# Kernel optimization log

Hardware: AMD Instinct MI355X
Metric: run time of the kernel (lower is better)

Reference implementation:

```python
import jax, jax.numpy as jnp
import numpy as np

B, S, T, H, E = 256, 512, 16, 1024, 512  # batch, src_len, trg_steps, hidden, emb_dim


def setup_inputs() -> dict:
    key = jax.random.key(0)
    ks = jax.random.split(key, 10)
    rn = lambda k, sh: jax.random.normal(k, sh, dtype=jnp.float32) * 0.05
    return {
        "trg_emb": rn(ks[0], (B, T, E)),
        "h0": rn(ks[1], (B, H)),
        "c0": rn(ks[2], (B, H)),
        "ctx": rn(ks[3], (B, S, H)),
        "src_len": jax.random.randint(ks[4], (B,), 1, S + 1, dtype=jnp.int32),
        "W_ih": rn(ks[5], (4 * H, E + H)),  # input-feeding: lstm in = emb + hidden
        "W_hh": rn(ks[6], (4 * H, H)),
        "b_ih": jnp.zeros((4 * H,), jnp.float32),
        "b_hh": jnp.zeros((4 * H,), jnp.float32),
        "W_in": rn(ks[7], (H, H)),    # attention linear_in (no bias)
        "W_out": rn(ks[8], (H, 2 * H)),  # attention linear_out (no bias)
    }


def reference(trg_emb, h0, c0, ctx, src_len, W_ih, W_hh, b_ih, b_hh, W_in, W_out):
    # mask[b, s] = s < src_len[b]
    mask = jnp.arange(S)[None, :] < src_len[:, None]  # (B, S)
    neg = jnp.float32(-1e9)

    def step(carry, emb_t):
        h, c, h_tilde = carry  # each (B, H); emb_t (B, E)
        # input feeding: concat target embedding with previous attentional vector
        x = jnp.concatenate([emb_t, h_tilde], axis=1)  # (B, E+H)
        gates = x @ W_ih.T + b_ih + h @ W_hh.T + b_hh  # (B, 4H), pytorch gate order i,f,g,o
        i, f, g, o = jnp.split(gates, 4, axis=1)
        i = jax.nn.sigmoid(i); f = jax.nn.sigmoid(f)
        g = jnp.tanh(g);       o = jax.nn.sigmoid(o)
        c = f * c + i * g
        h = o * jnp.tanh(c)
        # Luong soft-dot attention with src_len masking
        target = h @ W_in.T                                # (B, H)
        scores = jnp.einsum('bsh,bh->bs', ctx, target)     # (B, S)
        scores = jnp.where(mask, scores, neg)
        attn = jax.nn.softmax(scores, axis=-1)
        weighted = jnp.einsum('bs,bsh->bh', attn, ctx)     # (B, H)
        h_tilde = jnp.tanh(jnp.concatenate([weighted, h], axis=1) @ W_out.T)
        return (h, c, h_tilde), h_tilde

    # initial h_tilde = init_hidden[0] (per the original code)
    (h_f, c_f, _), hs = jax.lax.scan(step, (h0, c0, h0), jnp.swapaxes(trg_emb, 0, 1))
    output = jnp.swapaxes(hs, 0, 1)  # (B, T, H)
    return output, h_f, c_f
```

## Files before the change

kernel.cpp:

```cpp
#include <hip/hip_runtime.h>
#include <cstdint>
#include <cstddef>


#define B_ 256
#define S_ 512
#define T_ 16
#define H_ 1024
#define E_ 512

typedef unsigned short u16;
using short8 = __attribute__((ext_vector_type(8))) short;
using f32x4  = __attribute__((ext_vector_type(4))) float;

__device__ __forceinline__ float bf2f(u16 u) {
  union { uint32_t i; float f; } v; v.i = ((uint32_t)u) << 16; return v.f;
}
__device__ __forceinline__ u16 f2bf(float f) {
  union { uint32_t i; float f; } v; v.f = f;
  uint32_t r = v.i + 0x7fffu + ((v.i >> 16) & 1u);
  return (u16)(r >> 16);
}
__device__ __forceinline__ float sigmoidf_(float x) { return 1.f / (1.f + __expf(-x)); }

__device__ __forceinline__ void gload_lds16(const void* g, void* l) {
  __builtin_amdgcn_global_load_lds(
      (const __attribute__((address_space(1))) void*)g,
      (__attribute__((address_space(3))) void*)l, 16, 0, 0);
}

__global__ __launch_bounds__(256) void cvt_bf16(const float4* __restrict__ src,
                                                ushort4* __restrict__ dst, int n4) {
  for (int i = blockIdx.x * 256 + threadIdx.x; i < n4; i += gridDim.x * 256) {
    float4 v = src[i];
    ushort4 o; o.x = f2bf(v.x); o.y = f2bf(v.y); o.z = f2bf(v.z); o.w = f2bf(v.w);
    dst[i] = o;
  }
}

__global__ __launch_bounds__(256) void init_state(const float* __restrict__ h0,
                                                  const float* __restrict__ c0,
                                                  float* __restrict__ h32,
                                                  float* __restrict__ c,
                                                  u16* __restrict__ hbf,
                                                  u16* __restrict__ htbf) {
  int idx = blockIdx.x * 256 + threadIdx.x;
  float hv = h0[idx];
  h32[idx] = hv;
  c[idx] = c0[idx];
  u16 hb = f2bf(hv);
  hbf[idx] = hb;
  htbf[idx] = hb;
}

struct Region {
  const u16* A; int lda;
  const u16* Bw; int ldb;
  int klen;
};

template <int EPI>
__global__ __launch_bounds__(256) void gemm_ms(Region r0, Region r1, Region r2, int nreg,
                                               float* __restrict__ C, int ldc,
                                               u16* __restrict__ C2) {
  __shared__ u16 smA[2][128 * 64];
  __shared__ u16 smB[2][32 * 64];
  const int tid = threadIdx.x;
  const int lane = tid & 63;
  const int wave = tid >> 6;
  const int m0 = (blockIdx.x & 1) * 128;
  const int n0 = (blockIdx.x >> 1) * 32;

  Region rr[3] = { r0, r1, r2 };
  int tcnt[3];
  int nt = 0;
#pragma unroll
  for (int rg = 0; rg < 3; ++rg) { tcnt[rg] = (rg < nreg) ? (rr[rg].klen >> 6) : 0; nt += tcnt[rg]; }

  auto stage = [&](int lin, int buf) {
    int rg = 0, base = 0;
    while (lin >= base + tcnt[rg]) { base += tcnt[rg]; ++rg; }
    const int kr = (lin - base) << 6;
    const u16* A = rr[rg].A;  const int lda = rr[rg].lda;
    const u16* Bw = rr[rg].Bw; const int ldb = rr[rg].ldb;
#pragma unroll
    for (int j = 0; j < 4; ++j) {
      const int c = j * 256 + tid;
      const int row = c >> 3;
      const int q = (c & 7) ^ (row & 7);
      gload_lds16(A + (size_t)(m0 + row) * lda + kr + q * 8,
                  (char*)&smA[buf][0] + (size_t)(j * 256 + wave * 64) * 16);
    }
    {
      const int row = tid >> 3;
      const int q = (tid & 7) ^ (row & 7);
      gload_lds16(Bw + (size_t)(n0 + row) * ldb + kr + q * 8,
                  (char*)&smB[buf][0] + (size_t)(wave * 64) * 16);
    }
  };

  f32x4 acc[2][2] = {};
  stage(0, 0);
  for (int ti = 0; ti < nt; ++ti) {
    const int buf = ti & 1;
    __syncthreads();
    if (ti + 1 < nt) stage(ti + 1, buf ^ 1);
    const int row16 = lane & 15;
#pragma unroll
    for (int ks = 0; ks < 2; ++ks) {
      const int q = ks * 4 + (lane >> 4);
      short8 af[2], bfr[2];
#pragma unroll
      for (int mi = 0; mi < 2; ++mi) {
        const int R = wave * 32 + mi * 16 + row16;
        af[mi] = *(const short8*)((const char*)&smA[buf][0] + (size_t)(R * 8 + (q ^ (R & 7))) * 16);
      }
#pragma unroll
      for (int ni = 0; ni < 2; ++ni) {
        const int Rn = ni * 16 + row16;
        bfr[ni] = *(const short8*)((const char*)&smB[buf][0] + (size_t)(Rn * 8 + (q ^ (Rn & 7))) * 16);
      }
#pragma unroll
      for (int mi = 0; mi < 2; ++mi)
#pragma unroll
        for (int ni = 0; ni < 2; ++ni)
          acc[mi][ni] = __builtin_amdgcn_mfma_f32_16x16x32_bf16(af[mi], bfr[ni], acc[mi][ni], 0, 0, 0);
    }
  }
  const int row16 = lane & 15;
  const int kg = lane >> 4;
#pragma unroll
  for (int mi = 0; mi < 2; ++mi) {
#pragma unroll
    for (int ni = 0; ni < 2; ++ni) {
#pragma unroll
      for (int r = 0; r < 4; ++r) {
        const int row = m0 + wave * 32 + mi * 16 + kg * 4 + r;
        const int col = n0 + ni * 16 + row16;
        float v = acc[mi][ni][r];
        if (EPI == 0) {
          C[(size_t)row * ldc + col] = v;
        } else if (EPI == 1) {
          C2[row * H_ + col] = f2bf(v);
        } else {
          float tv = tanhf(v);
          C[(size_t)row * ldc + col] = tv;
          C2[row * H_ + col] = f2bf(tv);
        }
      }
    }
  }
}

__global__ __launch_bounds__(256) void lstm_pw(const float* __restrict__ gates,
                                               const float* __restrict__ b_ih,
                                               const float* __restrict__ b_hh,
                                               float* __restrict__ c,
                                               float* __restrict__ h32,
                                               u16* __restrict__ hbf) {
  const int idx = blockIdx.x * 256 + threadIdx.x;
  const int n = idx & (H_ - 1);
  const float* gb = gates + (size_t)(idx >> 10) * (4 * H_);
  float iv = gb[n]           + b_ih[n]           + b_hh[n];
  float fv = gb[H_ + n]      + b_ih[H_ + n]      + b_hh[H_ + n];
  float gv = gb[2 * H_ + n]  + b_ih[2 * H_ + n]  + b_hh[2 * H_ + n];
  float ov = gb[3 * H_ + n]  + b_ih[3 * H_ + n]  + b_hh[3 * H_ + n];
  iv = sigmoidf_(iv); fv = sigmoidf_(fv); gv = tanhf(gv); ov = sigmoidf_(ov);
  float cn = fv * c[idx] + iv * gv;
  c[idx] = cn;
  float hn = ov * tanhf(cn);
  h32[idx] = hn;
  hbf[idx] = f2bf(hn);
}

template <int ISBF>
__global__ __launch_bounds__(1024) void attn_on(const void* __restrict__ ctxv,
                                                const u16* __restrict__ target,
                                                const int* __restrict__ src_len,
                                                u16* __restrict__ wbf) {
  __shared__ float facc[16][1024];
  __shared__ float fm[16], fl[16];
  const int b = blockIdx.x;
  const int tid = threadIdx.x;
  const int lane = tid & 63;
  const int wave = tid >> 6;
  const int len = src_len[b];
  float tg[16];
  {
    const u16* tp = target + b * H_ + lane * 16;
    short8 v1 = *(const short8*)tp;
    short8 v2 = *(const short8*)(tp + 8);
#pragma unroll
    for (int j = 0; j < 8; ++j) { tg[j] = bf2f((u16)v1[j]); tg[8 + j] = bf2f((u16)v2[j]); }
  }
  float m = -1e30f, l = 0.f;
  float acc[16];
#pragma unroll
  for (int j = 0; j < 16; ++j) acc[j] = 0.f;

  for (int s = wave; s < len; s += 16) {
    float cf[16];
    if (ISBF) {
      const u16* cr = (const u16*)ctxv + (size_t)b * (S_ * H_) + (size_t)s * H_ + lane * 16;
      short8 v1 = *(const short8*)cr;
      short8 v2 = *(const short8*)(cr + 8);
#pragma unroll
      for (int j = 0; j < 8; ++j) { cf[j] = bf2f((u16)v1[j]); cf[8 + j] = bf2f((u16)v2[j]); }
    } else {
      const float* cr = (const float*)ctxv + (size_t)b * (S_ * H_) + (size_t)s * H_ + lane * 16;
      float4 w0 = *(const float4*)cr;
      float4 w1 = *(const float4*)(cr + 4);
      float4 w2 = *(const float4*)(cr + 8);
      float4 w3 = *(const float4*)(cr + 12);
      cf[0] = w0.x; cf[1] = w0.y; cf[2] = w0.z; cf[3] = w0.w;
      cf[4] = w1.x; cf[5] = w1.y; cf[6] = w1.z; cf[7] = w1.w;
      cf[8] = w2.x; cf[9] = w2.y; cf[10] = w2.z; cf[11] = w2.w;
      cf[12] = w3.x; cf[13] = w3.y; cf[14] = w3.z; cf[15] = w3.w;
    }
    float x = 0.f;
#pragma unroll
    for (int j = 0; j < 16; ++j) x += cf[j] * tg[j];
#pragma unroll
    for (int off = 1; off < 64; off <<= 1) x += __shfl_xor(x, off);
    if (x > m) {
      float sc_ = __expf(m - x);
      l *= sc_;
#pragma unroll
      for (int j = 0; j < 16; ++j) acc[j] *= sc_;
      m = x;
    }
    float p = __expf(x - m);
    l += p;
#pragma unroll
    for (int j = 0; j < 16; ++j) acc[j] += p * cf[j];
  }
  if (lane == 0) { fm[wave] = m; fl[wave] = l; }
#pragma unroll
  for (int j4 = 0; j4 < 4; ++j4) {
    float4 v;
    v.x = acc[j4 * 4]; v.y = acc[j4 * 4 + 1]; v.z = acc[j4 * 4 + 2]; v.w = acc[j4 * 4 + 3];
    *(float4*)&facc[wave][lane * 16 + j4 * 4] = v;
  }
  __syncthreads();
  float mstar = -1e30f;
#pragma unroll
  for (int w = 0; w < 16; ++w) mstar = fmaxf(mstar, fm[w]);
  float lsum = 0.f, asum = 0.f;
#pragma unroll
  for (int w = 0; w < 16; ++w) {
    float e = __expf(fm[w] - mstar);
    lsum += fl[w] * e;
    asum += facc[w][tid] * e;
  }
  wbf[b * H_ + tid] = f2bf(asum / lsum);
}

extern "C" void kernel_launch(void* const* d_in, const int* in_sizes, int n_in,
                              void* d_out, int out_size, void* d_ws, size_t ws_size,
                              hipStream_t stream) {
  const float* trg_emb = (const float*)d_in[0];
  const float* h0      = (const float*)d_in[1];
  const float* c0      = (const float*)d_in[2];
  const float* ctx     = (const float*)d_in[3];
  const int*   src_len = (const int*)d_in[4];
  const float* W_ih    = (const float*)d_in[5];
  const float* W_hh    = (const float*)d_in[6];
  const float* b_ih    = (const float*)d_in[7];
  const float* b_hh    = (const float*)d_in[8];
  const float* W_in    = (const float*)d_in[9];
  const float* W_out   = (const float*)d_in[10];
  float* out = (float*)d_out;

  char* w = (char*)d_ws;
  u16*   wWih  = (u16*)(w);
  u16*   wWhh  = (u16*)(w + 12582912);
  u16*   wWin  = (u16*)(w + 20971520);
  u16*   wWout = (u16*)(w + 23068672);
  u16*   wemb  = (u16*)(w + 27262976);
  float* wgates= (float*)(w + 31457280);
  float* wh32  = (float*)(w + 35651584);
  float* wc    = (float*)(w + 36700160);
  u16*   whbf  = (u16*)(w + 37748736);
  u16*   whtbf = (u16*)(w + 38273024);
  u16*   wtgt  = (u16*)(w + 38797312);
  u16*   wwbf  = (u16*)(w + 39321600);
  u16*   wctx  = (u16*)(w + 39845888);
  const bool ctx_bf = ws_size >= (size_t)39845888 + (size_t)268435456;

  auto cvt_launch = [&](const float* s, u16* d, int n) {
    int n4 = n / 4;
    int grid = (n4 + 255) / 256;
    if (grid > 4096) grid = 4096;
    cvt_bf16<<<dim3(grid), dim3(256), 0, stream>>>((const float4*)s, (ushort4*)d, n4);
  };
  cvt_launch(W_ih,  wWih,  4096 * 1536);
  cvt_launch(W_hh,  wWhh,  4096 * 1024);
  cvt_launch(W_in,  wWin,  1024 * 1024);
  cvt_launch(W_out, wWout, 1024 * 2048);
  cvt_launch(trg_emb, wemb, B_ * T_ * E_);
  if (ctx_bf) cvt_launch(ctx, wctx, B_ * S_ * H_);
  init_state<<<dim3((B_ * H_) / 256), dim3(256), 0, stream>>>(h0, c0, wh32, wc, whbf, whtbf);

  Region dummy = { nullptr, 0, nullptr, 0, 0 };
  for (int t = 0; t < T_; ++t) {
    Region g0 = { wemb + (size_t)t * E_, T_ * E_, wWih,      E_ + H_, E_ };
    Region g1 = { whtbf,                 H_,      wWih + E_, E_ + H_, H_ };
    Region g2 = { whbf,                  H_,      wWhh,      H_,      H_ };
    gemm_ms<0><<<dim3((4 * H_ / 32) * 2), dim3(256), 0, stream>>>(g0, g1, g2, 3, wgates, 4 * H_, (u16*)nullptr);
    lstm_pw<<<dim3((B_ * H_) / 256), dim3(256), 0, stream>>>(wgates, b_ih, b_hh, wc, wh32, whbf);
    Region i0 = { whbf, H_, wWin, H_, H_ };
    gemm_ms<1><<<dim3((H_ / 32) * 2), dim3(256), 0, stream>>>(i0, dummy, dummy, 1, (float*)nullptr, 0, wtgt);
    if (ctx_bf)
      attn_on<1><<<dim3(B_), dim3(1024), 0, stream>>>((const void*)wctx, wtgt, src_len, wwbf);
    else
      attn_on<0><<<dim3(B_), dim3(1024), 0, stream>>>((const void*)ctx, wtgt, src_len, wwbf);
    Region o0 = { wwbf, H_, wWout,      2 * H_, H_ };
    Region o1 = { whbf, H_, wWout + H_, 2 * H_, H_ };
    gemm_ms<2><<<dim3((H_ / 32) * 2), dim3(256), 0, stream>>>(o0, o1, dummy, 2,
                                                              out + (size_t)t * H_, T_ * H_, whtbf);
  }
  hipMemcpyAsync(out + (size_t)B_ * T_ * H_, wh32, (size_t)B_ * H_ * sizeof(float),
                 hipMemcpyDeviceToDevice, stream);
  hipMemcpyAsync(out + (size_t)B_ * T_ * H_ + B_ * H_, wc, (size_t)B_ * H_ * sizeof(float),
                 hipMemcpyDeviceToDevice, stream);
}
```

Measured before the change: 2.364 ms.

## Fuse LSTM pointwise into gate GEMM, fold linear_in into attention, merge conversions

Reorders the W_ih/W_hh rows so the four gates of each hidden unit sit next to each other. The gate GEMM epilogue can then apply bias and the LSTM cell update directly using lane shuffles, which removes the separate pointwise kernel and the fp32 gates round-trip. The W_in projection moves into the attention kernel as a per-batch GEMV on a transposed W_in, and the attention merge now reduces partials in two stages. All weight/input conversions and state init are combined into one kernel. The GEMMs use 64x64 tiles, 128 threads and 4-deep LDS buffering with manual waitcnts. The bf16 ctx copy is now always used regardless of workspace size, and the GEMM grids become much smaller (256 and 64 blocks), which may underfill the GPU.

Measured after the change: 2.237 ms. -5.4%, faster.

```diff
diff --git a/kernel.cpp b/kernel.cpp
--- a/kernel.cpp
+++ b/kernel.cpp
@@ -8,6 +8,7 @@
 #define T_ 16
 #define H_ 1024
 #define E_ 512
+#define NBUF 4
 
 typedef unsigned short u16;
 using short8 = __attribute__((ext_vector_type(8))) short;
@@ -29,194 +30,183 @@
       (__attribute__((address_space(3))) void*)l, 16, 0, 0);
 }
 
-__global__ __launch_bounds__(256) void cvt_bf16(const float4* __restrict__ src,
-                                                ushort4* __restrict__ dst, int n4) {
-  for (int i = blockIdx.x * 256 + threadIdx.x; i < n4; i += gridDim.x * 256) {
-    float4 v = src[i];
-    ushort4 o; o.x = f2bf(v.x); o.y = f2bf(v.y); o.z = f2bf(v.z); o.w = f2bf(v.w);
-    dst[i] = o;
-  }
-}
-
-__global__ __launch_bounds__(256) void init_state(const float* __restrict__ h0,
-                                                  const float* __restrict__ c0,
-                                                  float* __restrict__ h32,
-                                                  float* __restrict__ c,
-                                                  u16* __restrict__ hbf,
-                                                  u16* __restrict__ htbf) {
-  int idx = blockIdx.x * 256 + threadIdx.x;
-  float hv = h0[idx];
-  h32[idx] = hv;
-  c[idx] = c0[idx];
-  u16 hb = f2bf(hv);
-  hbf[idx] = hb;
-  htbf[idx] = hb;
-}
-
-struct Region {
-  const u16* A; int lda;
-  const u16* Bw; int ldb;
-  int klen;
-};
+struct Reg3 { const u16* A; int lda; const u16* B; int ldb; int kt; };
 
 template <int EPI>
-__global__ __launch_bounds__(256) void gemm_ms(Region r0, Region r1, Region r2, int nreg,
-                                               float* __restrict__ C, int ldc,
-                                               u16* __restrict__ C2) {
-  __shared__ u16 smA[2][128 * 64];
-  __shared__ u16 smB[2][32 * 64];
+__global__ __launch_bounds__(128) void gemm_k(Reg3 r0, Reg3 r1, Reg3 r2,
+                                              int nmb,
+                                              float* __restrict__ Cf,
+                                              u16* __restrict__ Cb,
+                                              const float* __restrict__ bsum,
+                                              float* __restrict__ cst,
+                                              float* __restrict__ h32o,
+                                              u16* __restrict__ hbfo,
+                                              const int tstep) {
+  __shared__ u16 smA[NBUF][64 * 64];
+  __shared__ u16 smB[NBUF][64 * 64];
   const int tid = threadIdx.x;
   const int lane = tid & 63;
   const int wave = tid >> 6;
-  const int m0 = (blockIdx.x & 1) * 128;
-  const int n0 = (blockIdx.x >> 1) * 32;
-
-  Region rr[3] = { r0, r1, r2 };
-  int tcnt[3];
-  int nt = 0;
-#pragma unroll
-  for (int rg = 0; rg < 3; ++rg) { tcnt[rg] = (rg < nreg) ? (rr[rg].klen >> 6) : 0; nt += tcnt[rg]; }
-
-  auto stage = [&](int lin, int buf) {
-    int rg = 0, base = 0;
-    while (lin >= base + tcnt[rg]) { base += tcnt[rg]; ++rg; }
-    const int kr = (lin - base) << 6;
-    const u16* A = rr[rg].A;  const int lda = rr[rg].lda;
-    const u16* Bw = rr[rg].Bw; const int ldb = rr[rg].ldb;
+  const int m0 = (blockIdx.x % nmb) * 64;
+  const int n0 = (blockIdx.x / nmb) * 64;
+  const int row16 = lane & 15;
+  const int kg = lane >> 4;
+  const int nt = r0.kt + r1.kt + r2.kt;
+
+  auto stage = [&](int ti, int buf) {
+    const int k01 = r0.kt + r1.kt;
+    const u16* Ap = (ti < r0.kt) ? r0.A : (ti < k01) ? r1.A : r2.A;
+    const u16* Bp = (ti < r0.kt) ? r0.B : (ti < k01) ? r1.B : r2.B;
+    const int lda = (ti < r0.kt) ? r0.lda : (ti < k01) ? r1.lda : r2.lda;
+    const int ldb = (ti < r0.kt) ? r0.ldb : (ti < k01) ? r1.ldb : r2.ldb;
+    const int base = (ti < r0.kt) ? 0 : (ti < k01) ? r0.kt : k01;
+    const int kr = (ti - base) << 6;
 #pragma unroll
     for (int j = 0; j < 4; ++j) {
-      const int c = j * 256 + tid;
-      const int row = c >> 3;
-      const int q = (c & 7) ^ (row & 7);
-      gload_lds16(A + (size_t)(m0 + row) * lda + kr + q * 8,
-                  (char*)&smA[buf][0] + (size_t)(j * 256 + wave * 64) * 16);
-    }
-    {
-      const int row = tid >> 3;
-      const int q = (tid & 7) ^ (row & 7);
-      gload_lds16(Bw + (size_t)(n0 + row) * ldb + kr + q * 8,
-                  (char*)&smB[buf][0] + (size_t)(wave * 64) * 16);
+      const int c = j * 128 + tid;
+      const int row = c >> 3, q = c & 7;
+      gload_lds16(Ap + (size_t)(m0 + row) * lda + kr + ((q ^ (row & 7)) << 3),
+                  (char*)&smA[buf][0] + (size_t)(j * 128 + wave * 64) * 16);
+    }
+#pragma unroll
+    for (int j = 0; j < 4; ++j) {
+      const int c = j * 128 + tid;
+      const int row = c >> 3, q = c & 7;
+      gload_lds16(Bp + (size_t)(n0 + row) * ldb + kr + ((q ^ (row & 7)) << 3),
+                  (char*)&smB[buf][0] + (size_t)(j * 128 + wave * 64) * 16);
     }
   };
 
-  f32x4 acc[2][2] = {};
+  f32x4 acc[4][2] = {};
   stage(0, 0);
+  if (nt > 1) stage(1, 1);
   for (int ti = 0; ti < nt; ++ti) {
-    const int buf = ti & 1;
-    __syncthreads();
-    if (ti + 1 < nt) stage(ti + 1, buf ^ 1);
-    const int row16 = lane & 15;
+    const int buf = ti & 3;
+    if (ti + 2 < nt) {
+      stage(ti + 2, (ti + 2) & 3);
+      asm volatile("s_waitcnt vmcnt(16)" ::: "memory");
+    } else if (ti + 1 < nt) {
+      asm volatile("s_waitcnt vmcnt(8)" ::: "memory");
+    } else {
+      asm volatile("s_waitcnt vmcnt(0)" ::: "memory");
+    }
+    __builtin_amdgcn_s_barrier();
+    __builtin_amdgcn_sched_barrier(0);
 #pragma unroll
     for (int ks = 0; ks < 2; ++ks) {
-      const int q = ks * 4 + (lane >> 4);
-      short8 af[2], bfr[2];
-#pragma unroll
-      for (int mi = 0; mi < 2; ++mi) {
-        const int R = wave * 32 + mi * 16 + row16;
-        af[mi] = *(const short8*)((const char*)&smA[buf][0] + (size_t)(R * 8 + (q ^ (R & 7))) * 16);
+      short8 af[4], bfr[2];
+#pragma unroll
+      for (int mi = 0; mi < 4; ++mi) {
+        const int R = mi * 16 + row16;
+        af[mi] = *(const short8*)((const char*)&smA[buf][0] +
+                                  (size_t)(((R << 3) | ((ks * 4 + kg) ^ (R & 7))) << 4));
       }
 #pragma unroll
       for (int ni = 0; ni < 2; ++ni) {
-        const int Rn = ni * 16 + row16;
-        bfr[ni] = *(const short8*)((const char*)&smB[buf][0] + (size_t)(Rn * 8 + (q ^ (Rn & 7))) * 16);
+        const int R = wave * 32 + ni * 16 + row16;
+        bfr[ni] = *(const short8*)((const char*)&smB[buf][0] +
+                                   (size_t)(((R << 3) | ((ks * 4 + kg) ^ (R & 7))) << 4));
       }
-#pragma unroll
-      for (int mi = 0; mi < 2; ++mi)
+      asm volatile("s_waitcnt lgkmcnt(0)" ::: "memory");
+      __builtin_amdgcn_sched_barrier(0);
+#pragma unroll
+      for (int mi = 0; mi < 4; ++mi)
 #pragma unroll
         for (int ni = 0; ni < 2; ++ni)
           acc[mi][ni] = __builtin_amdgcn_mfma_f32_16x16x32_bf16(af[mi], bfr[ni], acc[mi][ni], 0, 0, 0);
-    }
-  }
-  const int row16 = lane & 15;
-  const int kg = lane >> 4;
-#pragma unroll
-  for (int mi = 0; mi < 2; ++mi) {
+      __builtin_amdgcn_sched_barrier(0);
+    }
+  }
+#pragma unroll
+  for (int mi = 0; mi < 4; ++mi) {
 #pragma unroll
     for (int ni = 0; ni < 2; ++ni) {
 #pragma unroll
       for (int r = 0; r < 4; ++r) {
-        const int row = m0 + wave * 32 + mi * 16 + kg * 4 + r;
-        const int col = n0 + ni * 16 + row16;
+        const int row = m0 + mi * 16 + (kg << 2) + r;
+        const int col = n0 + wave * 32 + ni * 16 + row16;
         float v = acc[mi][ni][r];
-        if (EPI == 0) {
-          C[(size_t)row * ldc + col] = v;
-        } else if (EPI == 1) {
-          C2[row * H_ + col] = f2bf(v);
+        if (EPI == 2) {
+          float tv = tanhf(v);
+          Cf[(size_t)row * (T_ * H_) + (size_t)tstep * H_ + col] = tv;
+          Cb[row * H_ + col] = f2bf(tv);
         } else {
-          float tv = tanhf(v);
-          C[(size_t)row * ldc + col] = tv;
-          C2[row * H_ + col] = f2bf(tv);
+          v += bsum[col];
+          float v1 = __shfl_xor(v, 1);
+          float v2 = __shfl_xor(v, 2);
+          float v3 = __shfl_xor(v, 3);
+          if ((lane & 3) == 0) {
+            const int u = col >> 2;
+            float iv = sigmoidf_(v);
+            float fv = sigmoidf_(v1);
+            float gv = tanhf(v2);
+            float ov = sigmoidf_(v3);
+            float cn = fv * cst[row * H_ + u] + iv * gv;
+            float hn = ov * tanhf(cn);
+            cst[row * H_ + u] = cn;
+            h32o[row * H_ + u] = hn;
+            hbfo[row * H_ + u] = f2bf(hn);
+          }
         }
       }
     }
   }
 }
 
-__global__ __launch_bounds__(256) void lstm_pw(const float* __restrict__ gates,
-                                               const float* __restrict__ b_ih,
-                                               const float* __restrict__ b_hh,
-                                               float* __restrict__ c,
-                                               float* __restrict__ h32,
-                                               u16* __restrict__ hbf) {
-  const int idx = blockIdx.x * 256 + threadIdx.x;
-  const int n = idx & (H_ - 1);
-  const float* gb = gates + (size_t)(idx >> 10) * (4 * H_);
-  float iv = gb[n]           + b_ih[n]           + b_hh[n];
-  float fv = gb[H_ + n]      + b_ih[H_ + n]      + b_hh[H_ + n];
-  float gv = gb[2 * H_ + n]  + b_ih[2 * H_ + n]  + b_hh[2 * H_ + n];
-  float ov = gb[3 * H_ + n]  + b_ih[3 * H_ + n]  + b_hh[3 * H_ + n];
-  iv = sigmoidf_(iv); fv = sigmoidf_(fv); gv = tanhf(gv); ov = sigmoidf_(ov);
-  float cn = fv * c[idx] + iv * gv;
-  c[idx] = cn;
-  float hn = ov * tanhf(cn);
-  h32[idx] = hn;
-  hbf[idx] = f2bf(hn);
-}
-
-template <int ISBF>
-__global__ __launch_bounds__(1024) void attn_on(const void* __restrict__ ctxv,
-                                                const u16* __restrict__ target,
-                                                const int* __restrict__ src_len,
-                                                u16* __restrict__ wbf) {
-  __shared__ float facc[16][1024];
+__device__ __forceinline__ int fidx(int lane, int j) {
+  return (j << 6) + ((lane + (j << 2)) & 63);
+}
+
+__global__ __launch_bounds__(1024) void attn_k(const u16* __restrict__ hbf,
+                                               const u16* __restrict__ WinT,
+                                               const u16* __restrict__ ctxb,
+                                               const int* __restrict__ src_len,
+                                               u16* __restrict__ wwbf) {
+  __shared__ float hsm[1024];
+  __shared__ float tgtp[1024 + 64];
+  __shared__ float facc[8][1024];
   __shared__ float fm[16], fl[16];
   const int b = blockIdx.x;
   const int tid = threadIdx.x;
   const int lane = tid & 63;
   const int wave = tid >> 6;
   const int len = src_len[b];
+
+  hsm[tid] = bf2f(hbf[b * H_ + tid]);
+  __syncthreads();
+
+  {
+    float a = 0.f;
+    const u16* wp = WinT + tid * 8;
+    for (int k8 = 0; k8 < 128; ++k8) {
+      short8 wv = *(const short8*)(wp + (size_t)k8 * 8192);
+      float4 h0v = *(const float4*)&hsm[k8 * 8];
+      float4 h1v = *(const float4*)&hsm[k8 * 8 + 4];
+      a += bf2f((u16)wv[0]) * h0v.x + bf2f((u16)wv[1]) * h0v.y
+         + bf2f((u16)wv[2]) * h0v.z + bf2f((u16)wv[3]) * h0v.w
+         + bf2f((u16)wv[4]) * h1v.x + bf2f((u16)wv[5]) * h1v.y
+         + bf2f((u16)wv[6]) * h1v.z + bf2f((u16)wv[7]) * h1v.w;
+    }
+    tgtp[tid + (tid >> 4)] = a;
+  }
+  __syncthreads();
+
   float tg[16];
-  {
-    const u16* tp = target + b * H_ + lane * 16;
-    short8 v1 = *(const short8*)tp;
-    short8 v2 = *(const short8*)(tp + 8);
-#pragma unroll
-    for (int j = 0; j < 8; ++j) { tg[j] = bf2f((u16)v1[j]); tg[8 + j] = bf2f((u16)v2[j]); }
-  }
+#pragma unroll
+  for (int j = 0; j < 16; ++j) tg[j] = tgtp[lane * 17 + j];
+
   float m = -1e30f, l = 0.f;
   float acc[16];
 #pragma unroll
   for (int j = 0; j < 16; ++j) acc[j] = 0.f;
 
   for (int s = wave; s < len; s += 16) {
+    const u16* cr = ctxb + (((size_t)b * S_ + s) << 10) + (lane << 4);
+    short8 v1 = *(const short8*)cr;
+    short8 v2 = *(const short8*)(cr + 8);
     float cf[16];
-    if (ISBF) {
-      const u16* cr = (const u16*)ctxv + (size_t)b * (S_ * H_) + (size_t)s * H_ + lane * 16;
-      short8 v1 = *(const short8*)cr;
-      short8 v2 = *(const short8*)(cr + 8);
-#pragma unroll
-      for (int j = 0; j < 8; ++j) { cf[j] = bf2f((u16)v1[j]); cf[8 + j] = bf2f((u16)v2[j]); }
-    } else {
-      const float* cr = (const float*)ctxv + (size_t)b * (S_ * H_) + (size_t)s * H_ + lane * 16;
-      float4 w0 = *(const float4*)cr;
-      float4 w1 = *(const float4*)(cr + 4);
-      float4 w2 = *(const float4*)(cr + 8);
-      float4 w3 = *(const float4*)(cr + 12);
-      cf[0] = w0.x; cf[1] = w0.y; cf[2] = w0.z; cf[3] = w0.w;
-      cf[4] = w1.x; cf[5] = w1.y; cf[6] = w1.z; cf[7] = w1.w;
-      cf[8] = w2.x; cf[9] = w2.y; cf[10] = w2.z; cf[11] = w2.w;
-      cf[12] = w3.x; cf[13] = w3.y; cf[14] = w3.z; cf[15] = w3.w;
-    }
+#pragma unroll
+    for (int j = 0; j < 8; ++j) { cf[j] = bf2f((u16)v1[j]); cf[8 + j] = bf2f((u16)v2[j]); }
     float x = 0.f;
 #pragma unroll
     for (int j = 0; j < 16; ++j) x += cf[j] * tg[j];
@@ -234,25 +224,90 @@
 #pragma unroll
     for (int j = 0; j < 16; ++j) acc[j] += p * cf[j];
   }
-  if (lane == 0) { fm[wave] = m; fl[wave] = l; }
-#pragma unroll
-  for (int j4 = 0; j4 < 4; ++j4) {
-    float4 v;
-    v.x = acc[j4 * 4]; v.y = acc[j4 * 4 + 1]; v.z = acc[j4 * 4 + 2]; v.w = acc[j4 * 4 + 3];
-    *(float4*)&facc[wave][lane * 16 + j4 * 4] = v;
+
+  if (wave >= 8) {
+#pragma unroll
+    for (int j = 0; j < 16; ++j) facc[wave - 8][fidx(lane, j)] = acc[j];
+    if (lane == 0) { fm[wave] = m; fl[wave] = l; }
+  }
+  __syncthreads();
+  if (wave < 8) {
+    float pm = fm[8 + wave];
+    float pl = fl[8 + wave];
+    float M = fmaxf(m, pm);
+    float e1 = __expf(m - M);
+    float e2 = __expf(pm - M);
+#pragma unroll
+    for (int j = 0; j < 16; ++j) {
+      float pv = facc[wave][fidx(lane, j)];
+      facc[wave][fidx(lane, j)] = acc[j] * e1 + pv * e2;
+    }
+    if (lane == 0) { fm[wave] = M; fl[wave] = l * e1 + pl * e2; }
   }
   __syncthreads();
   float mstar = -1e30f;
 #pragma unroll
-  for (int w = 0; w < 16; ++w) mstar = fmaxf(mstar, fm[w]);
+  for (int w = 0; w < 8; ++w) mstar = fmaxf(mstar, fm[w]);
   float lsum = 0.f, asum = 0.f;
-#pragma unroll
-  for (int w = 0; w < 16; ++w) {
+  const int ri = fidx(tid >> 4, tid & 15);
+#pragma unroll
+  for (int w = 0; w < 8; ++w) {
     float e = __expf(fm[w] - mstar);
     lsum += fl[w] * e;
-    asum += facc[w][tid] * e;
-  }
-  wbf[b * H_ + tid] = f2bf(asum / lsum);
+    asum += facc[w][ri] * e;
+  }
+  wwbf[b * H_ + tid] = f2bf(asum / lsum);
+}
+
+__global__ __launch_bounds__(256) void convert_all(
+    const float* __restrict__ W_ih, const float* __restrict__ W_hh,
+    const float* __restrict__ W_in, const float* __restrict__ W_out,
+    const float* __restrict__ trg_emb, const float* __restrict__ ctx,
+    const float* __restrict__ b_ih, const float* __restrict__ b_hh,
+    const float* __restrict__ h0, const float* __restrict__ c0,
+    u16* __restrict__ wWih, u16* __restrict__ wWhh, u16* __restrict__ wWinT,
+    u16* __restrict__ wWout, u16* __restrict__ wemb, u16* __restrict__ wctx,
+    float* __restrict__ wbsum, u16* __restrict__ wh0, u16* __restrict__ whtbf,
+    float* __restrict__ wc) {
+  const int gtid = blockIdx.x * 256 + threadIdx.x;
+  const int GSZ = 2048 * 256;
+  auto cvt4 = [](float4 v) {
+    ushort4 o; o.x = f2bf(v.x); o.y = f2bf(v.y); o.z = f2bf(v.z); o.w = f2bf(v.w);
+    return o;
+  };
+  for (int i = gtid; i < 1572864; i += GSZ) {
+    const int r = i / 384, c4 = i - r * 384;
+    const int rp = ((r & 1023) << 2) + (r >> 10);
+    ((ushort4*)wWih)[(size_t)rp * 384 + c4] = cvt4(((const float4*)W_ih)[i]);
+  }
+  for (int i = gtid; i < 1048576; i += GSZ) {
+    const int r = i >> 8, c4 = i & 255;
+    const int rp = ((r & 1023) << 2) + (r >> 10);
+    ((ushort4*)wWhh)[(size_t)rp * 256 + c4] = cvt4(((const float4*)W_hh)[i]);
+  }
+  for (int i = gtid; i < 524288; i += GSZ)
+    ((ushort4*)wWout)[i] = cvt4(((const float4*)W_out)[i]);
+  for (int i = gtid; i < 524288; i += GSZ)
+    ((ushort4*)wemb)[i] = cvt4(((const float4*)trg_emb)[i]);
+  for (int i = gtid; i < 131072; i += GSZ) {
+    const int n = i >> 7, k8 = i & 127;
+    const float* s = W_in + (size_t)n * 1024 + k8 * 8;
+    ushort4* d = (ushort4*)(wWinT + (size_t)k8 * 8192 + n * 8);
+    d[0] = cvt4(*(const float4*)s);
+    d[1] = cvt4(*(const float4*)(s + 4));
+  }
+  for (int i = gtid; i < 33554432; i += GSZ)
+    ((ushort4*)wctx)[i] = cvt4(((const float4*)ctx)[i]);
+  if (gtid < 4096) {
+    const int cp = ((gtid & 1023) << 2) + (gtid >> 10);
+    wbsum[cp] = b_ih[gtid] + b_hh[gtid];
+  }
+  for (int i = gtid; i < 262144; i += GSZ) {
+    u16 hb = f2bf(h0[i]);
+    wh0[i] = hb;
+    whtbf[i] = hb;
+    wc[i] = c0[i];
+  }
 }
 
 extern "C" void kernel_launch(void* const* d_in, const int* in_sizes, int n_in,
@@ -272,52 +327,41 @@
   float* out = (float*)d_out;
 
   char* w = (char*)d_ws;
-  u16*   wWih  = (u16*)(w);
-  u16*   wWhh  = (u16*)(w + 12582912);
-  u16*   wWin  = (u16*)(w + 20971520);
-  u16*   wWout = (u16*)(w + 23068672);
-  u16*   wemb  = (u16*)(w + 27262976);
-  float* wgates= (float*)(w + 31457280);
-  float* wh32  = (float*)(w + 35651584);
-  float* wc    = (float*)(w + 36700160);
-  u16*   whbf  = (u16*)(w + 37748736);
-  u16*   whtbf = (u16*)(w + 38273024);
-  u16*   wtgt  = (u16*)(w + 38797312);
-  u16*   wwbf  = (u16*)(w + 39321600);
-  u16*   wctx  = (u16*)(w + 39845888);
-  const bool ctx_bf = ws_size >= (size_t)39845888 + (size_t)268435456;
-
-  auto cvt_launch = [&](const float* s, u16* d, int n) {
-    int n4 = n / 4;
-    int grid = (n4 + 255) / 256;
-    if (grid > 4096) grid = 4096;
-    cvt_bf16<<<dim3(grid), dim3(256), 0, stream>>>((const float4*)s, (ushort4*)d, n4);
-  };
-  cvt_launch(W_ih,  wWih,  4096 * 1536);
-  cvt_launch(W_hh,  wWhh,  4096 * 1024);
-  cvt_launch(W_in,  wWin,  1024 * 1024);
-  cvt_launch(W_out, wWout, 1024 * 2048);
-  cvt_launch(trg_emb, wemb, B_ * T_ * E_);
-  if (ctx_bf) cvt_launch(ctx, wctx, B_ * S_ * H_);
-  init_state<<<dim3((B_ * H_) / 256), dim3(256), 0, stream>>>(h0, c0, wh32, wc, whbf, whtbf);
-
-  Region dummy = { nullptr, 0, nullptr, 0, 0 };
+  size_t off = 0;
+  auto alloc = [&](size_t bytes) { char* p = w + off; off += bytes; return p; };
+  u16*   wWih  = (u16*)  alloc(12582912);
+  u16*   wWhh  = (u16*)  alloc(8388608);
+  u16*   wWinT = (u16*)  alloc(2097152);
+  u16*   wWout = (u16*)  alloc(4194304);
+  u16*   wemb  = (u16*)  alloc(4194304);
+  float* wbsum = (float*)alloc(16384);
+  float* wh32  = (float*)alloc(1048576);
+  float* wc    = (float*)alloc(1048576);
+  u16*   wh0   = (u16*)  alloc(524288);
+  u16*   wh1   = (u16*)  alloc(524288);
+  u16*   whtbf = (u16*)  alloc(524288);
+  u16*   wwbf  = (u16*)  alloc(524288);
+  u16*   wctx  = (u16*)  alloc(268435456);
+  (void)ws_size;
+
+  convert_all<<<dim3(2048), dim3(256), 0, stream>>>(
+      W_ih, W_hh, W_in, W_out, trg_emb, ctx, b_ih, b_hh, h0, c0,
+      wWih, wWhh, wWinT, wWout, wemb, wctx, wbsum, wh0, whtbf, wc);
+
+  Reg3 rz = { nullptr, 0, nullptr, 0, 0 };
   for (int t = 0; t < T_; ++t) {
-    Region g0 = { wemb + (size_t)t * E_, T_ * E_, wWih,      E_ + H_, E_ };
-    Region g1 = { whtbf,                 H_,      wWih + E_, E_ + H_, H_ };
-    Region g2 = { whbf,                  H_,      wWhh,      H_,      H_ };
-    gemm_ms<0><<<dim3((4 * H_ / 32) * 2), dim3(256), 0, stream>>>(g0, g1, g2, 3, wgates, 4 * H_, (u16*)nullptr);
-    lstm_pw<<<dim3((B_ * H_) / 256), dim3(256), 0, stream>>>(wgates, b_ih, b_hh, wc, wh32, whbf);
-    Region i0 = { whbf, H_, wWin, H_, H_ };
-    gemm_ms<1><<<dim3((H_ / 32) * 2), dim3(256), 0, stream>>>(i0, dummy, dummy, 1, (float*)nullptr, 0, wtgt);
-    if (ctx_bf)
-      attn_on<1><<<dim3(B_), dim3(1024), 0, stream>>>((const void*)wctx, wtgt, src_len, wwbf);
-    else
-      attn_on<0><<<dim3(B_), dim3(1024), 0, stream>>>((const void*)ctx, wtgt, src_len, wwbf);
-    Region o0 = { wwbf, H_, wWout,      2 * H_, H_ };
-    Region o1 = { whbf, H_, wWout + H_, 2 * H_, H_ };
-    gemm_ms<2><<<dim3((H_ / 32) * 2), dim3(256), 0, stream>>>(o0, o1, dummy, 2,
-                                                              out + (size_t)t * H_, T_ * H_, whtbf);
+    const u16* hcur = (t & 1) ? wh1 : wh0;
+    u16* hnxt = (t & 1) ? wh0 : wh1;
+    Reg3 g0 = { wemb + (size_t)t * E_, T_ * E_, wWih,      E_ + H_, 8 };
+    Reg3 g1 = { whtbf,                 H_,      wWih + E_, E_ + H_, 16 };
+    Reg3 g2 = { hcur,                  H_,      wWhh,      H_,      16 };
+    gemm_k<3><<<dim3(256), dim3(128), 0, stream>>>(
+        g0, g1, g2, 4, nullptr, nullptr, wbsum, wc, wh32, hnxt, 0);
+    attn_k<<<dim3(B_), dim3(1024), 0, stream>>>(hnxt, wWinT, wctx, src_len, wwbf);
+    Reg3 o0 = { wwbf, H_, wWout,      2 * H_, 16 };
+    Reg3 o1 = { hnxt, H_, wWout + H_, 2 * H_, 16 };
+    gemm_k<2><<<dim3(64), dim3(128), 0, stream>>>(
+        o0, o1, rz, 4, out, whtbf, nullptr, nullptr, nullptr, nullptr, t);
   }
   hipMemcpyAsync(out + (size_t)B_ * T_ * H_, wh32, (size_t)B_ * H_ * sizeof(float),
                  hipMemcpyDeviceToDevice, stream);
```
